# Kernel tuning notes

Hardware: AMD Instinct MI355X
Metric: run time of the kernel (lower is better)

## Reference

```python
import jax, jax.numpy as jnp
import numpy as np

N, IN_DIM, HID, OUT, E = 20000, 1024, 512, 128, 160000


def _xavier(key, fan_out, fan_in):
    a = (6.0 / (fan_in + fan_out)) ** 0.5
    return jax.random.uniform(key, (fan_out, fan_in), jnp.float32, -a, a)


def setup_inputs() -> dict:
    key = jax.random.key(0)
    ks = jax.random.split(key, 8)
    features = jax.random.normal(ks[0], (N, IN_DIM), jnp.float32)
    edge_index = jax.random.randint(ks[1], (2, E), 0, N, jnp.int64)
    W1 = _xavier(ks[2], HID, IN_DIM)   # conv1.lin.weight [out,in]
    b1 = jnp.zeros((HID,), jnp.float32)
    W2 = _xavier(ks[3], OUT, HID)      # conv2.lin.weight
    b2 = jnp.zeros((OUT,), jnp.float32)
    b3 = jnp.zeros((HID,), jnp.float32)  # conv3 bias (weight tied = W2.T)
    b4 = jnp.zeros((IN_DIM,), jnp.float32)  # conv4 bias (weight tied = W1.T)
    head1 = _xavier(ks[4], OUT, OUT)
    return dict(features=features, edge_index=edge_index, W1=W1, b1=b1,
                W2=W2, b2=b2, b3=b3, b4=b4, head1=head1)


def _gcn_conv(x, W, b, src, dst, norm, n):
    # GCNConv: transform then symmetric-normalized neighbor aggregation
    h = x @ W.T                       # [N, out]
    msg = h[src] * norm[:, None]      # [E', out] gathered + scaled
    out = jax.ops.segment_sum(msg, dst, num_segments=n)
    return out + b


def reference(features, edge_index, W1, b1, W2, b2, b3, b4, head1):
    n = features.shape[0]
    loops = jnp.arange(n, dtype=edge_index.dtype)
    src = jnp.concatenate([edge_index[0], loops])  # add self-loops
    dst = jnp.concatenate([edge_index[1], loops])
    deg = jax.ops.segment_sum(jnp.ones_like(dst, dtype=features.dtype), dst,
                              num_segments=n)
    dinv = jnp.where(deg > 0, deg ** -0.5, 0.0)
    norm = dinv[src] * dinv[dst]

    h1 = _gcn_conv(features, W1, b1, src, dst, norm, n)
    h2 = _gcn_conv(h1, W2, b2, src, dst, norm, n)
    z = h2 @ head1
    # tied weights: conv3.W = W2^T, conv4.W = W1^T
    h3 = _gcn_conv(z, W2.T, b3, src, dst, norm, n)
    h4 = _gcn_conv(h3, W1.T, b4, src, dst, norm, n)
    return z, h2, h4
```

## Files before the change

kernel.cpp:

```cpp
#include <hip/hip_runtime.h>

typedef short   short8  __attribute__((ext_vector_type(8)));
typedef unsigned short ushort8 __attribute__((ext_vector_type(8)));
typedef float   floatx4 __attribute__((ext_vector_type(4)));

__device__ __forceinline__ float bf2f(unsigned short h) {
    unsigned int u = ((unsigned int)h) << 16;
    return __builtin_bit_cast(float, u);
}
__device__ __forceinline__ unsigned short f2bf(float f) {
    unsigned int u = __builtin_bit_cast(unsigned int, f);
    u += 0x7fffu + ((u >> 16) & 1u);
    return (unsigned short)(u >> 16);
}


__global__ __launch_bounds__(256) void k_detect_f32(const unsigned short* __restrict__ X,
                                                    int nPairs, int* __restrict__ flags) {
    int i = blockIdx.x * 256 + threadIdx.x;
    if (i < nPairs) {
        unsigned short w = X[2 * i];
        if ((w & 0x7F80u) == 0x7F80u) atomicOr(&flags[0], 1);
    }
}

__global__ __launch_bounds__(256) void k_detect_i32(const int* __restrict__ ei,
                                                    int E, int* __restrict__ flags) {
    int i = blockIdx.x * 256 + threadIdx.x;
    if (i < E) {
        if (ei[2 * i + 1] != 0) atomicOr(&flags[1], 1);
    }
}


__global__ __launch_bounds__(256) void k_cvt_f32(const void* __restrict__ in,
                                                 float* __restrict__ out, int n,
                                                 const int* __restrict__ flags) {
    int i = blockIdx.x * 256 + threadIdx.x;
    if (i < n)
        out[i] = flags[0] ? ((const float*)in)[i] : bf2f(((const unsigned short*)in)[i]);
}

__global__ __launch_bounds__(256) void k_tcvt(const void* __restrict__ in,
                                              unsigned short* __restrict__ out,
                                              int R, int C, const int* __restrict__ flags) {
    int idx = blockIdx.x * 256 + threadIdx.x;
    if (idx >= R * C) return;
    int r = idx / C, c = idx - r * C;
    unsigned short v = flags[0] ? f2bf(((const float*)in)[idx])
                                : ((const unsigned short*)in)[idx];
    out[(long)c * R + r] = v;
}


__global__ __launch_bounds__(256) void k_count(const int* __restrict__ ei, int E, int n,
                                               const int* __restrict__ flags,
                                               int* __restrict__ deg) {
    int e = blockIdx.x * 256 + threadIdx.x;
    if (e >= E) return;
    int sh = (flags[1] == 0) ? 1 : 0;
    int d = ei[(long)(E + e) << sh];
    if ((unsigned)d < (unsigned)n) atomicAdd(&deg[d], 1);
}

__global__ __launch_bounds__(256) void k_dinv(const int* __restrict__ deg,
                                              float* __restrict__ dinv, int n) {
    int i = blockIdx.x * 256 + threadIdx.x;
    if (i < n) dinv[i] = rsqrtf((float)(deg[i] + 1));
}

__global__ __launch_bounds__(1024) void k_scan(const int* __restrict__ deg,
                                               int* __restrict__ row_start,
                                               int* __restrict__ cursor, int n) {
    __shared__ int sums[1024];
    int t = threadIdx.x;
    int CH = (n + 1 + 1023) / 1024;
    int base = t * CH;
    int s = 0;
    for (int i = 0; i < CH; i++) {
        int idx = base + i;
        if (idx < n) s += deg[idx];
    }
    sums[t] = s;
    __syncthreads();
    for (int off = 1; off < 1024; off <<= 1) {
        int v = (t >= off) ? sums[t - off] : 0;
        __syncthreads();
        if (t >= off) sums[t] += v;
        __syncthreads();
    }
    int run = (t > 0) ? sums[t - 1] : 0;
    for (int i = 0; i < CH; i++) {
        int idx = base + i;
        if (idx < n) {
            row_start[idx] = run;
            cursor[idx] = run;
            run += deg[idx];
        } else if (idx == n) {
            row_start[n] = run;
        }
    }
}

__global__ __launch_bounds__(256) void k_fill(const int* __restrict__ ei, int E, int n,
                                              const int* __restrict__ flags,
                                              int* __restrict__ cursor,
                                              int* __restrict__ csr) {
    int e = blockIdx.x * 256 + threadIdx.x;
    if (e >= E) return;
    int sh = (flags[1] == 0) ? 1 : 0;
    int s = ei[(long)e << sh];
    int d = ei[(long)(E + e) << sh];
    if ((unsigned)d >= (unsigned)n || (unsigned)s >= (unsigned)n) return;
    int p = atomicAdd(&cursor[d], 1);
    csr[p] = s;
}


__device__ __forceinline__ ushort8 ld8(const void* p, long e, bool f32) {
    if (!f32) return *(const ushort8*)((const unsigned short*)p + e);
    const float* f = (const float*)p + e;
    ushort8 r;
#pragma unroll
    for (int i = 0; i < 8; i++) r[i] = f2bf(f[i]);
    return r;
}

template <int BN>
__global__ __launch_bounds__(256, 2) void gemm_nt(const void* __restrict__ A, int aMaybeF32,
                                               const void* __restrict__ Bt, int bMaybeF32,
                                               void* __restrict__ Cv, long coff,
                                               const float* __restrict__ bias,
                                               int M, int N, int K, int finalOut,
                                               const int* __restrict__ flags) {
    constexpr int BM = 128, BK = 32, LDT = 40;
    constexpr int JR = BN / 16;
    __shared__ unsigned short sA[BM * LDT];
    __shared__ unsigned short sB[BN * LDT];
    const bool af32 = aMaybeF32 && flags[0];
    const bool bf32 = bMaybeF32 && flags[0];
    const bool of32 = finalOut && flags[0];
    const bool hasb = bias != nullptr;
    const int t = threadIdx.x;

    const int GX = gridDim.x;
    const int nwg = GX * gridDim.y;
    const int orig = blockIdx.y * GX + blockIdx.x;
    const int q8 = nwg >> 3, r8 = nwg & 7;
    const int xcd = orig & 7, cidx = orig >> 3;
    const int swz = (xcd < r8 ? xcd * (q8 + 1) : r8 * (q8 + 1) + (xcd - r8) * q8) + cidx;
    const int m0 = (swz / GX) * BM;
    const int n0 = (swz % GX) * BN;

    const int w = t >> 6;
    const int lane = t & 63;
    const int id = lane & 15;
    const int q = lane >> 4;

    floatx4 acc[2][JR];
#pragma unroll
    for (int s = 0; s < 2; s++)
#pragma unroll
        for (int j = 0; j < JR; j++) acc[s][j] = (floatx4)0.0f;

    const int ar = t >> 2;
    const int ac = (t & 3) * 8;

    for (int k0 = 0; k0 < K; k0 += BK) {
        long r0 = min(m0 + ar, M - 1);
        long r1 = min(m0 + ar + 64, M - 1);
        ushort8 va0 = ld8(A, r0 * K + k0 + ac, af32);
        ushort8 va1 = ld8(A, r1 * K + k0 + ac, af32);
        ushort8 vb0, vb1;
        vb0 = ld8(Bt, (long)min(n0 + ar, N - 1) * K + k0 + ac, bf32);
        if (BN == 128)
            vb1 = ld8(Bt, (long)min(n0 + ar + 64, N - 1) * K + k0 + ac, bf32);
        __syncthreads();
        *(ushort8*)(sA + ar * LDT + ac) = va0;
        *(ushort8*)(sA + (ar + 64) * LDT + ac) = va1;
        *(ushort8*)(sB + ar * LDT + ac) = vb0;
        if (BN == 128)
            *(ushort8*)(sB + (ar + 64) * LDT + ac) = vb1;
        __syncthreads();

        short8 afrag[2], bfrag[JR];
#pragma unroll
        for (int s = 0; s < 2; s++)
            afrag[s] = *(const short8*)(sA + (32 * w + 16 * s + id) * LDT + q * 8);
#pragma unroll
        for (int j = 0; j < JR; j++)
            bfrag[j] = *(const short8*)(sB + (16 * j + id) * LDT + q * 8);
#pragma unroll
        for (int s = 0; s < 2; s++)
#pragma unroll
            for (int j = 0; j < JR; j++)
                acc[s][j] = __builtin_amdgcn_mfma_f32_16x16x32_bf16(
                    afrag[s], bfrag[j], acc[s][j], 0, 0, 0);
    }

#pragma unroll
    for (int s = 0; s < 2; s++)
#pragma unroll
        for (int j = 0; j < JR; j++) {
            int col = n0 + 16 * j + id;
            float bv = hasb ? bias[col] : 0.0f;
#pragma unroll
            for (int r = 0; r < 4; r++) {
                int row = m0 + 32 * w + 16 * s + q * 4 + r;
                if (row < M) {
                    float v = acc[s][j][r] + bv;
                    if (of32) ((float*)Cv)[coff + (long)row * N + col] = v;
                    else ((unsigned short*)Cv)[coff + (long)row * N + col] = f2bf(v);
                }
            }
        }
}


template <int D>
__global__ __launch_bounds__(256) void k_agg(const unsigned short* __restrict__ T,
                                             const int* __restrict__ rs,
                                             const int* __restrict__ csr,
                                             const float* __restrict__ dinv,
                                             const float* __restrict__ bias,
                                             unsigned short* __restrict__ O, int n) {
    constexpr int TPN = D / 8;
    constexpr int NPB = 256 / TPN;
    int lt = threadIdx.x % TPN;
    int node = blockIdx.x * NPB + threadIdx.x / TPN;
    if (node >= n) return;
    int off = lt * 8;
    float acc[8];
#pragma unroll
    for (int i = 0; i < 8; i++) acc[i] = 0.0f;
    int beg = rs[node], end = rs[node + 1];
    for (int j = beg; j < end; j++) {
        int s = csr[j];
        if ((unsigned)s >= (unsigned)n) continue;
        float wgt = dinv[s];
        ushort8 v = *(const ushort8*)(T + (long)s * D + off);
#pragma unroll
        for (int i = 0; i < 8; i++) acc[i] += wgt * bf2f(v[i]);
    }
    float di = dinv[node];
    ushort8 sv = *(const ushort8*)(T + (long)node * D + off);
    ushort8 o;
#pragma unroll
    for (int i = 0; i < 8; i++) {
        float r = di * (acc[i] + di * bf2f(sv[i])) + (bias ? bias[off + i] : 0.0f);
        o[i] = f2bf(r);
    }
    *(ushort8*)(O + (long)node * D + off) = o;
}


__global__ __launch_bounds__(256) void k_out(const unsigned short* __restrict__ z,
                                             const unsigned short* __restrict__ h2,
                                             void* __restrict__ out, int nOut,
                                             const int* __restrict__ flags) {
    int i = blockIdx.x * 256 + threadIdx.x;
    if (i >= 2 * nOut) return;
    unsigned short v = (i < nOut) ? z[i] : h2[i - nOut];
    if (flags[0]) ((float*)out)[i] = bf2f(v);
    else ((unsigned short*)out)[i] = v;
}


extern "C" void kernel_launch(void* const* d_in, const int* in_sizes, int n_in,
                              void* d_out, int out_size, void* d_ws, size_t ws_size,
                              hipStream_t stream) {
    const int IN  = in_sizes[7];
    const int HID = in_sizes[3];
    const int OUT = in_sizes[5];
    const int Nn  = in_sizes[0] / IN;
    const int E   = in_sizes[1] / 2;

    const void* X   = d_in[0];
    const int*  ei  = (const int*)d_in[1];
    const void* W1  = d_in[2];
    const void* b1  = d_in[3];
    const void* W2  = d_in[4];
    const void* b2  = d_in[5];
    const void* b3  = d_in[6];
    const void* b4  = d_in[7];
    const void* Hd1 = d_in[8];

    char* base = (char*)d_ws;
    size_t o = 0;
    auto carve = [&](size_t bytes) -> char* {
        char* p = base + o;
        o = (o + bytes + 255) & ~(size_t)255;
        return p;
    };
    int*   flags  = (int*)carve(2 * 4);
    int*   deg    = (int*)carve((size_t)Nn * 4);
    int*   rowst  = (int*)carve((size_t)(Nn + 1) * 4);
    int*   cursor = (int*)carve((size_t)Nn * 4);
    float* dinv   = (float*)carve((size_t)Nn * 4);
    int*   csr    = (int*)carve((size_t)E * 4);
    float* biasf  = (float*)carve((size_t)(HID + OUT + HID + IN) * 4);
    float* bc1 = biasf, *bc2 = biasf + HID, *bc3 = biasf + HID + OUT,
         *bc4 = biasf + HID + OUT + HID;
    unsigned short* W1t  = (unsigned short*)carve((size_t)IN * HID * 2);
    unsigned short* W2t  = (unsigned short*)carve((size_t)HID * OUT * 2);
    unsigned short* H1t  = (unsigned short*)carve((size_t)OUT * OUT * 2);
    unsigned short* t1   = (unsigned short*)carve((size_t)Nn * HID * 2);
    unsigned short* h1   = (unsigned short*)carve((size_t)Nn * HID * 2);
    unsigned short* h3   = (unsigned short*)carve((size_t)Nn * HID * 2);
    unsigned short* t2   = (unsigned short*)carve((size_t)Nn * OUT * 2);
    unsigned short* h2ws = (unsigned short*)carve((size_t)Nn * OUT * 2);
    unsigned short* zws  = (unsigned short*)carve((size_t)Nn * OUT * 2);

    hipMemsetAsync(flags, 0, 8, stream);
    hipMemsetAsync(deg, 0, (size_t)Nn * 4, stream);
    int nPairs = 1 << 20;
    k_detect_f32<<<(nPairs + 255) / 256, 256, 0, stream>>>((const unsigned short*)X, nPairs, flags);
    k_detect_i32<<<(E + 255) / 256, 256, 0, stream>>>(ei, E, flags);

    k_cvt_f32<<<(HID + 255) / 256, 256, 0, stream>>>(b1, bc1, HID, flags);
    k_cvt_f32<<<(OUT + 255) / 256, 256, 0, stream>>>(b2, bc2, OUT, flags);
    k_cvt_f32<<<(HID + 255) / 256, 256, 0, stream>>>(b3, bc3, HID, flags);
    k_cvt_f32<<<(IN + 255) / 256, 256, 0, stream>>>(b4, bc4, IN, flags);

    k_tcvt<<<(HID * IN + 255) / 256, 256, 0, stream>>>(W1, W1t, HID, IN, flags);
    k_tcvt<<<(OUT * HID + 255) / 256, 256, 0, stream>>>(W2, W2t, OUT, HID, flags);
    k_tcvt<<<(OUT * OUT + 255) / 256, 256, 0, stream>>>(Hd1, H1t, OUT, OUT, flags);

    k_count<<<(E + 255) / 256, 256, 0, stream>>>(ei, E, Nn, flags, deg);
    k_dinv<<<(Nn + 255) / 256, 256, 0, stream>>>(deg, dinv, Nn);
    k_scan<<<1, 1024, 0, stream>>>(deg, rowst, cursor, Nn);
    k_fill<<<(E + 255) / 256, 256, 0, stream>>>(ei, E, Nn, flags, cursor, csr);

    dim3 blk(256);
    auto ggrid = [&](int Ncols, int bn) { return dim3((Ncols + bn - 1) / bn, (Nn + 127) / 128); };
    const long zOff = 0, h2Off = (long)Nn * OUT, h4Off = (long)Nn * OUT * 2;

    gemm_nt<128><<<ggrid(HID, 128), blk, 0, stream>>>(X, 1, W1, 1, t1, 0, nullptr, Nn, HID, IN, 0, flags);
    k_agg<512><<<(Nn * 64 + 255) / 256, blk, 0, stream>>>(t1, rowst, csr, dinv, bc1, h1, Nn);

    gemm_nt<64><<<ggrid(OUT, 64), blk, 0, stream>>>(h1, 0, W2, 1, t2, 0, nullptr, Nn, OUT, HID, 0, flags);
    k_agg<128><<<(Nn * 16 + 255) / 256, blk, 0, stream>>>(t2, rowst, csr, dinv, bc2, h2ws, Nn);

    gemm_nt<64><<<ggrid(OUT, 64), blk, 0, stream>>>(h2ws, 0, H1t, 0, zws, 0, nullptr, Nn, OUT, OUT, 0, flags);

    k_agg<128><<<(Nn * 16 + 255) / 256, blk, 0, stream>>>(zws, rowst, csr, dinv, nullptr, t2, Nn);
    gemm_nt<128><<<ggrid(HID, 128), blk, 0, stream>>>(t2, 0, W2t, 0, h3, 0, bc3, Nn, HID, OUT, 0, flags);

    k_agg<512><<<(Nn * 64 + 255) / 256, blk, 0, stream>>>(h3, rowst, csr, dinv, nullptr, t1, Nn);
    gemm_nt<128><<<ggrid(IN, 128), blk, 0, stream>>>(t1, 0, W1t, 0, d_out, h4Off, bc4, Nn, IN, HID, 1, flags);

    k_out<<<(2 * (int)h2Off + 255) / 256, blk, 0, stream>>>(zws, h2ws, d_out, (int)h2Off, flags);
}
```

Before: 601.2 us.

## Pre-convert features and weights to bf16 and simplify GEMM loads

Adds a vectorized conversion kernel that turns X, W1 and W2 into bf16 copies once, up front. The GEMM then always reads bf16 with plain vector loads instead of branching on fp32 and converting element by element inside the inner loop. The launch bounds rise to 3 blocks per CU, and two GEMMs switch from a 128-wide to a 64-wide N tile. The cost is an extra full pass over X (20000x1024) and a separate bf16 buffer for it. The narrower tiles also mean more blocks, with A tiles reloaded more often.

```diff
diff --git a/kernel.cpp b/kernel.cpp
--- a/kernel.cpp
+++ b/kernel.cpp
@@ -39,6 +39,23 @@
     int i = blockIdx.x * 256 + threadIdx.x;
     if (i < n)
         out[i] = flags[0] ? ((const float*)in)[i] : bf2f(((const unsigned short*)in)[i]);
+}
+
+__global__ __launch_bounds__(256) void k_cvt8(const void* __restrict__ in,
+                                              unsigned short* __restrict__ out,
+                                              long n8, const int* __restrict__ flags) {
+    long i = (long)blockIdx.x * 256 + threadIdx.x;
+    if (i >= n8) return;
+    ushort8 o;
+    if (flags[0]) {
+        const floatx4* f = (const floatx4*)in + i * 2;
+        floatx4 a = f[0], b = f[1];
+#pragma unroll
+        for (int j = 0; j < 4; j++) { o[j] = f2bf(a[j]); o[4 + j] = f2bf(b[j]); }
+    } else {
+        o = *((const ushort8*)in + i);
+    }
+    *((ushort8*)out + i) = o;
 }
 
 __global__ __launch_bounds__(256) void k_tcvt(const void* __restrict__ in,
@@ -117,18 +134,9 @@
 }
 
 
-__device__ __forceinline__ ushort8 ld8(const void* p, long e, bool f32) {
-    if (!f32) return *(const ushort8*)((const unsigned short*)p + e);
-    const float* f = (const float*)p + e;
-    ushort8 r;
-#pragma unroll
-    for (int i = 0; i < 8; i++) r[i] = f2bf(f[i]);
-    return r;
-}
-
 template <int BN>
-__global__ __launch_bounds__(256, 2) void gemm_nt(const void* __restrict__ A, int aMaybeF32,
-                                               const void* __restrict__ Bt, int bMaybeF32,
+__global__ __launch_bounds__(256, 3) void gemm_nt(const unsigned short* __restrict__ A,
+                                               const unsigned short* __restrict__ Bt,
                                                void* __restrict__ Cv, long coff,
                                                const float* __restrict__ bias,
                                                int M, int N, int K, int finalOut,
@@ -137,8 +145,6 @@
     constexpr int JR = BN / 16;
     __shared__ unsigned short sA[BM * LDT];
     __shared__ unsigned short sB[BN * LDT];
-    const bool af32 = aMaybeF32 && flags[0];
-    const bool bf32 = bMaybeF32 && flags[0];
     const bool of32 = finalOut && flags[0];
     const bool hasb = bias != nullptr;
     const int t = threadIdx.x;
@@ -169,18 +175,21 @@
     for (int k0 = 0; k0 < K; k0 += BK) {
         long r0 = min(m0 + ar, M - 1);
         long r1 = min(m0 + ar + 64, M - 1);
-        ushort8 va0 = ld8(A, r0 * K + k0 + ac, af32);
-        ushort8 va1 = ld8(A, r1 * K + k0 + ac, af32);
+        ushort8 va0 = *(const ushort8*)(A + r0 * K + k0 + ac);
+        ushort8 va1 = *(const ushort8*)(A + r1 * K + k0 + ac);
         ushort8 vb0, vb1;
-        vb0 = ld8(Bt, (long)min(n0 + ar, N - 1) * K + k0 + ac, bf32);
+        vb0 = *(const ushort8*)(Bt + (long)min(n0 + ar, N - 1) * K + k0 + ac);
         if (BN == 128)
-            vb1 = ld8(Bt, (long)min(n0 + ar + 64, N - 1) * K + k0 + ac, bf32);
+            vb1 = *(const ushort8*)(Bt + (long)min(n0 + ar + 64, N - 1) * K + k0 + ac);
         __syncthreads();
         *(ushort8*)(sA + ar * LDT + ac) = va0;
         *(ushort8*)(sA + (ar + 64) * LDT + ac) = va1;
-        *(ushort8*)(sB + ar * LDT + ac) = vb0;
-        if (BN == 128)
+        if (BN == 128) {
+            *(ushort8*)(sB + ar * LDT + ac) = vb0;
             *(ushort8*)(sB + (ar + 64) * LDT + ac) = vb1;
+        } else {
+            if (ar < 64) *(ushort8*)(sB + ar * LDT + ac) = vb0;
+        }
         __syncthreads();
 
         short8 afrag[2], bfrag[JR];
@@ -304,6 +313,9 @@
     unsigned short* W1t  = (unsigned short*)carve((size_t)IN * HID * 2);
     unsigned short* W2t  = (unsigned short*)carve((size_t)HID * OUT * 2);
     unsigned short* H1t  = (unsigned short*)carve((size_t)OUT * OUT * 2);
+    unsigned short* W1c  = (unsigned short*)carve((size_t)HID * IN * 2);
+    unsigned short* W2c  = (unsigned short*)carve((size_t)OUT * HID * 2);
+    unsigned short* Xb   = (unsigned short*)carve((size_t)Nn * IN * 2);
     unsigned short* t1   = (unsigned short*)carve((size_t)Nn * HID * 2);
     unsigned short* h1   = (unsigned short*)carve((size_t)Nn * HID * 2);
     unsigned short* h3   = (unsigned short*)carve((size_t)Nn * HID * 2);
@@ -326,6 +338,15 @@
     k_tcvt<<<(OUT * HID + 255) / 256, 256, 0, stream>>>(W2, W2t, OUT, HID, flags);
     k_tcvt<<<(OUT * OUT + 255) / 256, 256, 0, stream>>>(Hd1, H1t, OUT, OUT, flags);
 
+    {
+        long n8x = (long)Nn * IN / 8;
+        k_cvt8<<<(int)((n8x + 255) / 256), 256, 0, stream>>>(X, Xb, n8x, flags);
+        long n8w1 = (long)HID * IN / 8;
+        k_cvt8<<<(int)((n8w1 + 255) / 256), 256, 0, stream>>>(W1, W1c, n8w1, flags);
+        long n8w2 = (long)OUT * HID / 8;
+        k_cvt8<<<(int)((n8w2 + 255) / 256), 256, 0, stream>>>(W2, W2c, n8w2, flags);
+    }
+
     k_count<<<(E + 255) / 256, 256, 0, stream>>>(ei, E, Nn, flags, deg);
     k_dinv<<<(Nn + 255) / 256, 256, 0, stream>>>(deg, dinv, Nn);
     k_scan<<<1, 1024, 0, stream>>>(deg, rowst, cursor, Nn);
@@ -335,19 +356,19 @@
     auto ggrid = [&](int Ncols, int bn) { return dim3((Ncols + bn - 1) / bn, (Nn + 127) / 128); };
     const long zOff = 0, h2Off = (long)Nn * OUT, h4Off = (long)Nn * OUT * 2;
 
-    gemm_nt<128><<<ggrid(HID, 128), blk, 0, stream>>>(X, 1, W1, 1, t1, 0, nullptr, Nn, HID, IN, 0, flags);
+    gemm_nt<64><<<ggrid(HID, 64), blk, 0, stream>>>(Xb, W1c, t1, 0, nullptr, Nn, HID, IN, 0, flags);
     k_agg<512><<<(Nn * 64 + 255) / 256, blk, 0, stream>>>(t1, rowst, csr, dinv, bc1, h1, Nn);
 
-    gemm_nt<64><<<ggrid(OUT, 64), blk, 0, stream>>>(h1, 0, W2, 1, t2, 0, nullptr, Nn, OUT, HID, 0, flags);
+    gemm_nt<64><<<ggrid(OUT, 64), blk, 0, stream>>>(h1, W2c, t2, 0, nullptr, Nn, OUT, HID, 0, flags);
     k_agg<128><<<(Nn * 16 + 255) / 256, blk, 0, stream>>>(t2, rowst, csr, dinv, bc2, h2ws, Nn);
 
-    gemm_nt<64><<<ggrid(OUT, 64), blk, 0, stream>>>(h2ws, 0, H1t, 0, zws, 0, nullptr, Nn, OUT, OUT, 0, flags);
+    gemm_nt<64><<<ggrid(OUT, 64), blk, 0, stream>>>(h2ws, H1t, zws, 0, nullptr, Nn, OUT, OUT, 0, flags);
 
     k_agg<128><<<(Nn * 16 + 255) / 256, blk, 0, stream>>>(zws, rowst, csr, dinv, nullptr, t2, Nn);
-    gemm_nt<128><<<ggrid(HID, 128), blk, 0, stream>>>(t2, 0, W2t, 0, h3, 0, bc3, Nn, HID, OUT, 0, flags);
+    gemm_nt<64><<<ggrid(HID, 64), blk, 0, stream>>>(t2, W2t, h3, 0, bc3, Nn, HID, OUT, 0, flags);
 
     k_agg<512><<<(Nn * 64 + 255) / 256, blk, 0, stream>>>(h3, rowst, csr, dinv, nullptr, t1, Nn);
-    gemm_nt<128><<<ggrid(IN, 128), blk, 0, stream>>>(t1, 0, W1t, 0, d_out, h4Off, bc4, Nn, IN, HID, 1, flags);
+    gemm_nt<128><<<ggrid(IN, 128), blk, 0, stream>>>(t1, W1t, d_out, h4Off, bc4, Nn, IN, HID, 1, flags);
 
     k_out<<<(2 * (int)h2Off + 255) / 256, blk, 0, stream>>>(zws, h2ws, d_out, (int)h2Off, flags);
 }
```

New measurement: 572.6 us. -4.8%, faster.
